# Optimization experiments

Hardware: AMD Instinct MI355X
Metric: run time of the kernel (lower is better)

The kernel has to match this reference:

```python
import jax, jax.numpy as jnp
import numpy as np

TEMPLATE_SUBDIVISION = 8
SIGMA = 0.5
NORMALISED = True


def setup_inputs() -> dict:
    key = jax.random.key(0)
    k1, k2, k3 = jax.random.split(key, 3)
    B, N, M_full, D = 2, 32768, 8192, 3
    x = jax.random.normal(k1, (B, N, D), dtype=jnp.float32)
    deformed_verts = jax.random.normal(k2, (B, M_full, D), dtype=jnp.float32)
    mean_shape_verts = jax.random.normal(k3, (B, M_full, D), dtype=jnp.float32)
    deformation_parameters = jnp.zeros((1,), dtype=jnp.float32)  # unused by transform
    return {
        "x": x,
        "deformed_verts": deformed_verts,
        "mean_shape_verts": mean_shape_verts,
        "deformation_parameters": deformation_parameters,
    }


def reference(x, deformed_verts, mean_shape_verts, deformation_parameters):
    # subsample template vertices: [B, M_full, D] -> [B, M, D]
    dv = deformed_verts[:, ::TEMPLATE_SUBDIVISION]
    mv = mean_shape_verts[:, ::TEMPLATE_SUBDIVISION]
    inv_sigma2 = 1.0 / (SIGMA ** 2)
    # broadcast RBF-like kernel: [B, M, N, D]
    kernel_res = jnp.exp(-jnp.abs(x[:, None, :, :] - dv[:, :, None, :]) * inv_sigma2)
    # weighted sum over control vertices M -> [B, N, D]
    out = jnp.sum(mv[:, :, None, :] * kernel_res, axis=1)
    if NORMALISED:
        denominator = jnp.sum(kernel_res, axis=1)
        out = out / denominator
    return out
```

## Files before the change

kernel.cpp:

```cpp
#include <hip/hip_runtime.h>
#include <math.h>

constexpr int B       = 2;
constexpr int N       = 32768;
constexpr int D       = 3;
constexpr int M_FULL  = 8192;
constexpr int SUBDIV  = 8;
constexpr int M       = M_FULL / SUBDIV;
constexpr int K       = 512;
constexpr float LO    = -4.0f;
constexpr float INV_W = 64.0f;
constexpr int BLOCK   = 256;
constexpr int CHUNKS  = N / BLOCK;
constexpr float K4    = 5.770780163555852f;

__device__ inline void scan512_pre(float* a) {
    const int lane = threadIdx.x & 63;
    const int base = lane * 8;
    float xv[8], e[8];
    float ls = 0.f;
    #pragma unroll
    for (int t = 0; t < 8; ++t) xv[t] = a[base + t];
    #pragma unroll
    for (int t = 0; t < 8; ++t) { e[t] = ls; ls += xv[t]; }
    float inc = ls;
    #pragma unroll
    for (int off = 1; off < 64; off <<= 1) {
        const float tmp = __shfl_up(inc, off, 64);
        if (lane >= off) inc += tmp;
    }
    const float exoff = inc - ls;
    #pragma unroll
    for (int t = 0; t < 8; ++t) a[base + t] = exoff + e[t];
}

__device__ inline void scan512_suf(float* a) {
    const int lane = threadIdx.x & 63;
    const int base = lane * 8;
    float xv[8], e[8];
    float ls = 0.f;
    #pragma unroll
    for (int t = 0; t < 8; ++t) xv[t] = a[base + t];
    #pragma unroll
    for (int t = 7; t >= 0; --t) { e[t] = ls; ls += xv[t]; }
    float inc = ls;
    #pragma unroll
    for (int off = 1; off < 64; off <<= 1) {
        const float tmp = __shfl_down(inc, off, 64);
        if (lane + off < 64) inc += tmp;
    }
    const float exoff = inc - ls;
    #pragma unroll
    for (int t = 0; t < 8; ++t) a[base + t] = exoff + e[t] + xv[t];
}

__device__ inline void scan512_i(const int* cntA, int* begA, int* curA) {
    const int lane = threadIdx.x & 63;
    const int base = lane * 8;
    int xv[8], e[8];
    int ls = 0;
    #pragma unroll
    for (int t = 0; t < 8; ++t) xv[t] = cntA[base + t];
    #pragma unroll
    for (int t = 0; t < 8; ++t) { e[t] = ls; ls += xv[t]; }
    int inc = ls;
    #pragma unroll
    for (int off = 1; off < 64; off <<= 1) {
        const int tmp = __shfl_up(inc, off, 64);
        if (lane >= off) inc += tmp;
    }
    const int exoff = inc - ls;
    #pragma unroll
    for (int t = 0; t < 8; ++t) {
        begA[base + t] = exoff + e[t];
        curA[base + t] = exoff + e[t];
    }
}

__global__ __launch_bounds__(BLOCK) void deformer_one(
    const float* __restrict__ x,
    const float* __restrict__ dverts,
    const float* __restrict__ mverts,
    float* __restrict__ out)
{
    __shared__ float sV[M], sAp[M], sSp[M], sAm[M], sSm[M];
    __shared__ float gAp[K], gSp[K], gAm[K], gSm[K];
    __shared__ int   cnt[K], beg[K], cur[K];

    const int tid = threadIdx.x;
    const int p = blockIdx.x >> 7;
    const int c = blockIdx.x & 127;
    const int b = p / 3, d = p % 3;

    for (int i = tid; i < K; i += BLOCK) {
        cnt[i] = 0; gAp[i] = 0.f; gSp[i] = 0.f; gAm[i] = 0.f; gSm[i] = 0.f;
    }
    __syncthreads();

    float vv[4], ap[4], sp[4], am[4], sm[4]; int bj[4];
    #pragma unroll
    for (int u = 0; u < 4; ++u) {
        const int i = tid + u * BLOCK;
        const int g = (b * M_FULL + i * SUBDIV) * D + d;
        const float v = dverts[g];
        const float w = mverts[g];
        const float epv = __builtin_amdgcn_exp2f( K4 * v);
        const float emv = __builtin_amdgcn_exp2f(-K4 * v);
        vv[u] = v;
        ap[u] = w * epv; sp[u] = epv;
        am[u] = w * emv; sm[u] = emv;
        int j = (int)floorf((v - LO) * INV_W);
        j = j < 0 ? 0 : (j > K - 1 ? K - 1 : j);
        bj[u] = j;
        atomicAdd(&cnt[j], 1);
        atomicAdd(&gAp[j], ap[u]);
        atomicAdd(&gSp[j], sp[u]);
        atomicAdd(&gAm[j], am[u]);
        atomicAdd(&gSm[j], sm[u]);
    }
    __syncthreads();

    const int wid = tid >> 6;
    if (wid == 0) { scan512_i(cnt, beg, cur); scan512_suf(gSm); }
    else if (wid == 1) scan512_pre(gAp);
    else if (wid == 2) scan512_pre(gSp);
    else               scan512_suf(gAm);
    __syncthreads();

    #pragma unroll
    for (int u = 0; u < 4; ++u) {
        const int pos = atomicAdd(&cur[bj[u]], 1);
        sV[pos] = vv[u]; sAp[pos] = ap[u]; sSp[pos] = sp[u];
        sAm[pos] = am[u]; sSm[pos] = sm[u];
    }
    __syncthreads();

    const int n = c * BLOCK + tid;
    const int o = (b * N + n) * D + d;
    const float xq = x[o];

    int j = (int)floorf((xq - LO) * INV_W);
    j = j < 0 ? 0 : (j > K - 1 ? K - 1 : j);

    const float en  = __builtin_amdgcn_exp2f(-K4 * xq);
    const float epx = __builtin_amdgcn_exp2f( K4 * xq);

    float Ap = gAp[j];
    float Sp = gSp[j];
    float Am = (j < K - 1) ? gAm[j + 1] : 0.f;
    float Sm = (j < K - 1) ? gSm[j + 1] : 0.f;

    const int s0 = beg[j], s1 = s0 + cnt[j];
    float rAp = 0.f, rSp = 0.f, rAm = 0.f, rSm = 0.f;
    for (int i = s0; i < s1; ++i) {
        const bool le = (sV[i] <= xq);
        rAp += le ? sAp[i] : 0.f;
        rSp += le ? sSp[i] : 0.f;
        rAm += le ? 0.f : sAm[i];
        rSm += le ? 0.f : sSm[i];
    }
    out[o] = (en * (Ap + rAp) + epx * (Am + rAm)) /
             (en * (Sp + rSp) + epx * (Sm + rSm));
}

extern "C" void kernel_launch(void* const* d_in, const int* in_sizes, int n_in,
                              void* d_out, int out_size, void* d_ws, size_t ws_size,
                              hipStream_t stream) {
    const float* x  = (const float*)d_in[0];
    const float* dv = (const float*)d_in[1];
    const float* mv = (const float*)d_in[2];
    float* out = (float*)d_out;

    deformer_one<<<B * D * CHUNKS, BLOCK, 0, stream>>>(x, dv, mv, out);
}
```

Measured before the change: 79.19 us.

## Build per-pair tables once and share via cooperative grid sync

Instead of every block rebuilding the sorted template tables and prefix sums, only the first block per (batch, dim) pair builds them and writes them to global workspace. After a grid-wide cooperative sync, the other blocks copy the tables into shared memory and run the query. This removes redundant atomics and scans across 128 blocks per pair, at the cost of a grid sync, a global round trip, and a cooperative launch that falls back to the old kernel on failure.

After: 176.6 us. 2.23x slower.

```diff
diff --git a/kernel.cpp b/kernel.cpp
--- a/kernel.cpp
+++ b/kernel.cpp
@@ -1,5 +1,8 @@
 #include <hip/hip_runtime.h>
+#include <hip/hip_cooperative_groups.h>
 #include <math.h>
+
+namespace cg = cooperative_groups;
 
 constexpr int B       = 2;
 constexpr int N       = 32768;
@@ -12,13 +15,15 @@
 constexpr float INV_W = 64.0f;
 constexpr int BLOCK   = 256;
 constexpr int CHUNKS  = N / BLOCK;
+constexpr int GRID    = B * D * CHUNKS;
 constexpr float K4    = 5.770780163555852f;
+
+constexpr int TSTRIDE = 8192;
 
 __device__ inline void scan512_pre(float* a) {
     const int lane = threadIdx.x & 63;
     const int base = lane * 8;
-    float xv[8], e[8];
-    float ls = 0.f;
+    float xv[8], e[8]; float ls = 0.f;
     #pragma unroll
     for (int t = 0; t < 8; ++t) xv[t] = a[base + t];
     #pragma unroll
@@ -37,8 +42,7 @@
 __device__ inline void scan512_suf(float* a) {
     const int lane = threadIdx.x & 63;
     const int base = lane * 8;
-    float xv[8], e[8];
-    float ls = 0.f;
+    float xv[8], e[8]; float ls = 0.f;
     #pragma unroll
     for (int t = 0; t < 8; ++t) xv[t] = a[base + t];
     #pragma unroll
@@ -57,8 +61,7 @@
 __device__ inline void scan512_i(const int* cntA, int* begA, int* curA) {
     const int lane = threadIdx.x & 63;
     const int base = lane * 8;
-    int xv[8], e[8];
-    int ls = 0;
+    int xv[8], e[8]; int ls = 0;
     #pragma unroll
     for (int t = 0; t < 8; ++t) xv[t] = cntA[base + t];
     #pragma unroll
@@ -77,21 +80,15 @@
     }
 }
 
-__global__ __launch_bounds__(BLOCK) void deformer_one(
-    const float* __restrict__ x,
-    const float* __restrict__ dverts,
-    const float* __restrict__ mverts,
-    float* __restrict__ out)
-{
-    __shared__ float sV[M], sAp[M], sSp[M], sAm[M], sSm[M];
-    __shared__ float gAp[K], gSp[K], gAm[K], gSm[K];
-    __shared__ int   cnt[K], beg[K], cur[K];
-
+__device__ inline void build_tables(const float* __restrict__ dverts,
+                                    const float* __restrict__ mverts,
+                                    int b, int d,
+                                    float* sV, float* sAp, float* sSp,
+                                    float* sAm, float* sSm,
+                                    float* gAp, float* gSp, float* gAm, float* gSm,
+                                    int* cnt, int* beg, int* cur)
+{
     const int tid = threadIdx.x;
-    const int p = blockIdx.x >> 7;
-    const int c = blockIdx.x & 127;
-    const int b = p / 3, d = p % 3;
-
     for (int i = tid; i < K; i += BLOCK) {
         cnt[i] = 0; gAp[i] = 0.f; gSp[i] = 0.f; gAm[i] = 0.f; gSm[i] = 0.f;
     }
@@ -121,7 +118,7 @@
     __syncthreads();
 
     const int wid = tid >> 6;
-    if (wid == 0) { scan512_i(cnt, beg, cur); scan512_suf(gSm); }
+    if (wid == 0)      { scan512_i(cnt, beg, cur); scan512_suf(gSm); }
     else if (wid == 1) scan512_pre(gAp);
     else if (wid == 2) scan512_pre(gSp);
     else               scan512_suf(gAm);
@@ -134,7 +131,18 @@
         sAm[pos] = am[u]; sSm[pos] = sm[u];
     }
     __syncthreads();
-
+}
+
+__device__ inline void run_query(const float* __restrict__ x,
+                                 float* __restrict__ out,
+                                 int b, int d, int c,
+                                 const float* sV, const float* sAp, const float* sSp,
+                                 const float* sAm, const float* sSm,
+                                 const float* gAp, const float* gSp,
+                                 const float* gAm, const float* gSm,
+                                 const int* cnt, const int* beg)
+{
+    const int tid = threadIdx.x;
     const int n = c * BLOCK + tid;
     const int o = (b * N + n) * D + d;
     const float xq = x[o];
@@ -145,10 +153,10 @@
     const float en  = __builtin_amdgcn_exp2f(-K4 * xq);
     const float epx = __builtin_amdgcn_exp2f( K4 * xq);
 
-    float Ap = gAp[j];
-    float Sp = gSp[j];
-    float Am = (j < K - 1) ? gAm[j + 1] : 0.f;
-    float Sm = (j < K - 1) ? gSm[j + 1] : 0.f;
+    const float Ap = gAp[j];
+    const float Sp = gSp[j];
+    const float Am = (j < K - 1) ? gAm[j + 1] : 0.f;
+    const float Sm = (j < K - 1) ? gSm[j + 1] : 0.f;
 
     const int s0 = beg[j], s1 = s0 + cnt[j];
     float rAp = 0.f, rSp = 0.f, rAm = 0.f, rSm = 0.f;
@@ -163,6 +171,76 @@
              (en * (Sp + rSp) + epx * (Sm + rSm));
 }
 
+__global__ __launch_bounds__(BLOCK) void deformer_coop(
+    const float* __restrict__ x,
+    const float* __restrict__ dverts,
+    const float* __restrict__ mverts,
+    float* __restrict__ out,
+    float* __restrict__ tab)
+{
+    __shared__ __align__(16) float lds[TSTRIDE + K];
+    float* sV  = lds;          float* sAp = lds + 1024;
+    float* sSp = lds + 2048;   float* sAm = lds + 3072;
+    float* sSm = lds + 4096;
+    float* gAp = lds + 5120;   float* gSp = lds + 5632;
+    float* gAm = lds + 6144;   float* gSm = lds + 6656;
+    int*   beg = (int*)(lds + 7168);
+    int*   cnt = (int*)(lds + 7680);
+    int*   cur = (int*)(lds + TSTRIDE);
+
+    const int tid = threadIdx.x;
+    const int p = blockIdx.x >> 7;
+    const int c = blockIdx.x & 127;
+    const int b = p / 3, d = p % 3;
+    float* tp = tab + p * TSTRIDE;
+
+    if (c == 0) {
+        build_tables(dverts, mverts, b, d, sV, sAp, sSp, sAm, sSm,
+                     gAp, gSp, gAm, gSm, cnt, beg, cur);
+        for (int i = tid; i < 2048; i += BLOCK)
+            reinterpret_cast<float4*>(tp)[i] =
+                reinterpret_cast<const float4*>(lds)[i];
+    }
+
+    cg::this_grid().sync();
+
+    if (c != 0) {
+        for (int i = tid; i < 2048; i += BLOCK)
+            reinterpret_cast<float4*>(lds)[i] =
+                reinterpret_cast<const float4*>(tp)[i];
+        __syncthreads();
+    }
+
+    run_query(x, out, b, d, c, sV, sAp, sSp, sAm, sSm,
+              gAp, gSp, gAm, gSm, cnt, beg);
+}
+
+__global__ __launch_bounds__(BLOCK) void deformer_one(
+    const float* __restrict__ x,
+    const float* __restrict__ dverts,
+    const float* __restrict__ mverts,
+    float* __restrict__ out)
+{
+    __shared__ __align__(16) float lds[TSTRIDE + K];
+    float* sV  = lds;          float* sAp = lds + 1024;
+    float* sSp = lds + 2048;   float* sAm = lds + 3072;
+    float* sSm = lds + 4096;
+    float* gAp = lds + 5120;   float* gSp = lds + 5632;
+    float* gAm = lds + 6144;   float* gSm = lds + 6656;
+    int*   beg = (int*)(lds + 7168);
+    int*   cnt = (int*)(lds + 7680);
+    int*   cur = (int*)(lds + TSTRIDE);
+
+    const int p = blockIdx.x >> 7;
+    const int c = blockIdx.x & 127;
+    const int b = p / 3, d = p % 3;
+
+    build_tables(dverts, mverts, b, d, sV, sAp, sSp, sAm, sSm,
+                 gAp, gSp, gAm, gSm, cnt, beg, cur);
+    run_query(x, out, b, d, c, sV, sAp, sSp, sAm, sSm,
+              gAp, gSp, gAm, gSm, cnt, beg);
+}
+
 extern "C" void kernel_launch(void* const* d_in, const int* in_sizes, int n_in,
                               void* d_out, int out_size, void* d_ws, size_t ws_size,
                               hipStream_t stream) {
@@ -170,6 +248,13 @@
     const float* dv = (const float*)d_in[1];
     const float* mv = (const float*)d_in[2];
     float* out = (float*)d_out;
-
-    deformer_one<<<B * D * CHUNKS, BLOCK, 0, stream>>>(x, dv, mv, out);
-}
+    float* tab = (float*)d_ws;
+
+    void* args[] = { (void*)&x, (void*)&dv, (void*)&mv, (void*)&out, (void*)&tab };
+    hipError_t e = hipLaunchCooperativeKernel(
+        reinterpret_cast<void*>(deformer_coop),
+        dim3(GRID), dim3(BLOCK), args, 0, stream);
+    if (e != hipSuccess) {
+        deformer_one<<<GRID, BLOCK, 0, stream>>>(x, dv, mv, out);
+    }
+}
```
